# Kernel tuning notes

Hardware: AMD Instinct MI355X
Metric: run time of the kernel (lower is better)

Reference implementation:

```python
import jax, jax.numpy as jnp
import numpy as np

N_HEAD = 16
N_EMBD = 1024
SEQ = 2048
BATCH = 4


def setup_inputs() -> dict:
    key = jax.random.key(0)
    ks = jax.random.split(key, 5)
    s_in = 1.0 / np.sqrt(N_EMBD)
    return {
        "x": jax.random.normal(ks[0], (BATCH, SEQ, N_EMBD), dtype=jnp.float32),
        "W_attn": jax.random.normal(ks[1], (N_EMBD, 3 * N_EMBD), dtype=jnp.float32) * s_in,
        "b_attn": jax.random.normal(ks[2], (3 * N_EMBD,), dtype=jnp.float32) * 0.01,
        "W_proj": jax.random.normal(ks[3], (N_EMBD, N_EMBD), dtype=jnp.float32) * s_in,
        "b_proj": jax.random.normal(ks[4], (N_EMBD,), dtype=jnp.float32) * 0.01,
    }


def reference(x, W_attn, b_attn, W_proj, b_proj):
    B, T, C = x.shape
    H = N_HEAD
    D = C // H  # head dim
    qkv = x @ W_attn + b_attn                      # [B,T,3C]
    q, k, v = jnp.split(qkv, 3, axis=-1)
    # [B,T,C] -> [B,H,T,D]
    q = q.reshape(B, T, H, D).transpose(0, 2, 1, 3)
    k = k.reshape(B, T, H, D).transpose(0, 2, 1, 3)
    v = v.reshape(B, T, H, D).transpose(0, 2, 1, 3)
    scale = 1.0 / np.sqrt(D).astype(np.float32)
    att = jnp.einsum('bhqd,bhkd->bhqk', q, k) * scale   # [B,H,T,T]
    causal = jnp.tril(jnp.ones((T, T), dtype=bool))
    att = jnp.where(causal, att, jnp.finfo(att.dtype).min)
    att = jax.nn.softmax(att, axis=-1)
    y = jnp.einsum('bhqk,bhkd->bhqd', att, v)            # [B,H,T,D]
    y = y.transpose(0, 2, 1, 3).reshape(B, T, C)
    return y @ W_proj + b_proj
```

## Files before the change

kernel.cpp:

```cpp
#include <hip/hip_runtime.h>
#include <stdint.h>

typedef __attribute__((ext_vector_type(8))) short short8;
typedef __attribute__((ext_vector_type(4))) short short4v;
typedef __attribute__((ext_vector_type(4))) float f32x4;
typedef __attribute__((ext_vector_type(2))) unsigned int uint2v;

#define B_ 4
#define T_ 2048
#define C_ 1024
#define H_ 16
#define D_ 64
#define C3_ 3072

#define AS1 __attribute__((address_space(1)))
#define AS3 __attribute__((address_space(3)))

#define QK_SCALE 0.18033688f

__device__ __forceinline__ unsigned short f2bf(float f) {
    union { float f; uint32_t u; } v; v.f = f;
    uint32_t r = v.u + 0x7FFFu + ((v.u >> 16) & 1u);
    return (unsigned short)(r >> 16);
}

__device__ __forceinline__ uint32_t pk_bf16(float lo, float hi) {
    uint32_t r;
    asm("v_cvt_pk_bf16_f32 %0, %1, %2" : "=v"(r) : "v"(lo), "v"(hi));
    return r;
}

__global__ void k_cvt_bf16(const float* __restrict__ in, unsigned short* __restrict__ out, int n4) {
    int i = blockIdx.x * blockDim.x + threadIdx.x;
    if (i >= n4) return;
    float4 v = ((const float4*)in)[i];
    unsigned short o0 = f2bf(v.x), o1 = f2bf(v.y), o2 = f2bf(v.z), o3 = f2bf(v.w);
    unsigned long long packed = (unsigned long long)o0 | ((unsigned long long)o1 << 16)
        | ((unsigned long long)o2 << 32) | ((unsigned long long)o3 << 48);
    *(unsigned long long*)(out + (size_t)i * 4) = packed;
}

__global__ void k_wtrans(const float* __restrict__ W, unsigned short* __restrict__ WT, int K, int N) {
    __shared__ float t[32][33];
    int n0 = blockIdx.x * 32, k0 = blockIdx.y * 32;
    int tx = threadIdx.x, ty = threadIdx.y;
#pragma unroll
    for (int i = 0; i < 4; ++i)
        t[ty + i * 8][tx] = W[(size_t)(k0 + ty + i * 8) * N + n0 + tx];
    __syncthreads();
#pragma unroll
    for (int i = 0; i < 4; ++i)
        WT[(size_t)(n0 + ty + i * 8) * K + k0 + tx] = f2bf(t[tx][ty + i * 8]);
}

__global__ void k_prep_vt(const unsigned short* __restrict__ qkv, unsigned short* __restrict__ vt) {
    int bh = blockIdx.y; int b = bh >> 4, h = bh & 15;
    int t0 = blockIdx.x * 64;
    __shared__ unsigned short tile[64][72];
    int tid = threadIdx.x;
    int r = tid >> 3;
    int c = (tid & 7) * 8;
#pragma unroll
    for (int rr = 0; rr < 64; rr += 32) {
        const unsigned short* src = qkv + (size_t)(b * T_ + t0 + r + rr) * C3_ + 2 * C_ + h * D_ + c;
        short8 v = *(const short8*)src;
#pragma unroll
        for (int j = 0; j < 8; ++j) tile[r + rr][c + j] = (unsigned short)v[j];
    }
    __syncthreads();
#pragma unroll
    for (int rr = 0; rr < 64; rr += 32) {
        int d = r + rr;
        short8 sv;
#pragma unroll
        for (int j = 0; j < 8; ++j) sv[j] = (short)tile[c + j][d];
        *(short8*)(vt + (size_t)bh * D_ * T_ + (size_t)d * T_ + t0 + c) = sv;
    }
}

template<bool OUT_BF16>
__global__ __launch_bounds__(512) void k_gemm_bt(const unsigned short* __restrict__ A,
                                                 const unsigned short* __restrict__ BT,
                                                 const float* __restrict__ bias,
                                                 unsigned short* __restrict__ outb,
                                                 float* __restrict__ outf,
                                                 int M, int N, int K) {
    __shared__ __align__(16) char arena[147456];
    int tid = threadIdx.x;
    int w = tid >> 6, lane = tid & 63;
    int wrow = w >> 1, wcol = w & 1;
    int m0 = blockIdx.y * 256, n0 = blockIdx.x * 128;
    int lr = lane & 15, lg = lane >> 4;

    f32x4 acc[4][4] = {};

    int gr = tid >> 3;
    int scb = ((tid & 7) << 4) ^ (((tid >> 3) & 7) << 4);
    const char* sA[4];
    const char* sB[2];
#pragma unroll
    for (int r = 0; r < 4; ++r)
        sA[r] = (const char*)A + (size_t)(m0 + gr + r * 64) * K * 2 + scb;
#pragma unroll
    for (int r = 0; r < 2; ++r)
        sB[r] = (const char*)BT + (size_t)(n0 + gr + r * 64) * K * 2 + scb;

    int inner = (lg * 16) ^ ((lr & 7) << 4);
    int aoff = wrow * 8192 + lr * 128 + inner;
    int boff = 32768 + wcol * 8192 + lr * 128 + inner;

#define GSTAGE(OFS)                                                                                 \
    {                                                                                               \
        _Pragma("unroll")                                                                           \
        for (int r = 0; r < 4; ++r) {                                                               \
            __builtin_amdgcn_global_load_lds((const AS1 void*)sA[r],                                \
                (AS3 void*)(arena + (OFS) + tid * 16 + r * 8192), 16, 0, 0);                        \
            sA[r] += 128;                                                                           \
        }                                                                                           \
        _Pragma("unroll")                                                                           \
        for (int r = 0; r < 2; ++r) {                                                               \
            __builtin_amdgcn_global_load_lds((const AS1 void*)sB[r],                                \
                (AS3 void*)(arena + (OFS) + 32768 + tid * 16 + r * 8192), 16, 0, 0);                \
            sB[r] += 128;                                                                           \
        }                                                                                           \
    }

#define GCOMPUTE(OFS)                                                                               \
    {                                                                                               \
        short8 af[4][2], bf[4][2];                                                                  \
        _Pragma("unroll")                                                                           \
        for (int i = 0; i < 4; ++i) {                                                               \
            int addrA = (OFS) + aoff + i * 2048;                                                    \
            af[i][0] = *(const short8*)(arena + addrA);                                             \
            af[i][1] = *(const short8*)(arena + (addrA ^ 64));                                      \
        }                                                                                           \
        _Pragma("unroll")                                                                           \
        for (int j = 0; j < 4; ++j) {                                                               \
            int addrB = (OFS) + boff + j * 2048;                                                    \
            bf[j][0] = *(const short8*)(arena + addrB);                                             \
            bf[j][1] = *(const short8*)(arena + (addrB ^ 64));                                      \
        }                                                                                           \
        __builtin_amdgcn_s_setprio(1);                                                              \
        _Pragma("unroll")                                                                           \
        for (int i = 0; i < 4; ++i)                                                                 \
            _Pragma("unroll")                                                                       \
            for (int j = 0; j < 4; ++j) {                                                           \
                acc[i][j] = __builtin_amdgcn_mfma_f32_16x16x32_bf16(af[i][0], bf[j][0], acc[i][j], 0, 0, 0); \
                acc[i][j] = __builtin_amdgcn_mfma_f32_16x16x32_bf16(af[i][1], bf[j][1], acc[i][j], 0, 0, 0); \
            }                                                                                       \
        __builtin_amdgcn_s_setprio(0);                                                              \
    }

    int NT = K >> 6;
    int ofs0 = 0, ofs1 = 49152, ofs2 = 98304;

    GSTAGE(ofs0);
    GSTAGE(ofs1);
    asm volatile("s_waitcnt vmcnt(6)" ::: "memory");
    __builtin_amdgcn_s_barrier();
    __builtin_amdgcn_sched_barrier(0);

    for (int t = 0; t < NT; ++t) {
        bool pf = (t + 2 < NT);
        if (pf) GSTAGE(ofs2);
        GCOMPUTE(ofs0);
        if (pf) { asm volatile("s_waitcnt vmcnt(6)" ::: "memory"); }
        else    { asm volatile("s_waitcnt vmcnt(0)" ::: "memory"); }
        __builtin_amdgcn_s_barrier();
        __builtin_amdgcn_sched_barrier(0);
        int tmp = ofs0; ofs0 = ofs1; ofs1 = ofs2; ofs2 = tmp;
    }
#undef GSTAGE
#undef GCOMPUTE

#pragma unroll
    for (int i = 0; i < 4; ++i) {
        int row = m0 + wrow * 64 + i * 16 + lg * 4;
#pragma unroll
        for (int j = 0; j < 4; ++j) {
            int col = n0 + wcol * 64 + j * 16 + lr;
            float bv = bias[col];
#pragma unroll
            for (int r = 0; r < 4; ++r) {
                float v = acc[i][j][r] + bv;
                if (OUT_BF16) {
                    if (col < C_) v *= QK_SCALE;
                    outb[(size_t)(row + r) * N + col] = f2bf(v);
                } else {
                    outf[(size_t)(row + r) * N + col] = v;
                }
            }
        }
    }
}

__global__ __launch_bounds__(256, 4) void k_attn(const unsigned short* __restrict__ qkv,
                                                 const unsigned short* __restrict__ vt,
                                                 unsigned short* __restrict__ y) {
    __shared__ __align__(16) char arena[40960];
    int tid = threadIdx.x;
    int w = tid >> 6, lane = tid & 63;
    int lr = lane & 15, lg = lane >> 4;

    int bid = blockIdx.x;
    int bid2 = (bid & 7) * 128 + (bid >> 3);
    int bh = bid2 >> 4, pair = bid2 & 15;
    int b = bh >> 4, h = bh & 15;

    const unsigned short* kbase = qkv + (size_t)(b * T_) * C3_ + C_ + h * D_;
    const unsigned short* vtb = vt + (size_t)bh * D_ * T_;

    int sw_ = (lr & 7) << 4;
    int RB0 = lr * 128 + ((lg * 16) ^ sw_);
    int RB1 = RB0 ^ 64;
    int jl = (lr >> 1) & 3;
    int pbase = 32768 + w * 2048 + lr * 128
              + ((((lg >> 1) ^ (lr & 1)) << 4) | (((lg & 1) ^ (lr >> 3)) << 3));
    int pwa[4];
#pragma unroll
    for (int j = 0; j < 4; ++j) pwa[j] = pbase + ((j ^ jl) << 5);
    int prd0 = 32768 + w * 2048 + lr * 128 + ((lg ^ (lr & 7)) << 4);
    int prd1 = prd0 ^ 64;
    int hs = lr & 8;
    int prA0a = prd0 + hs,       prA0b = prd0 + (8 ^ hs);
    int prA1a = prd1 + hs,       prA1b = prd1 + (8 ^ hs);

    int row0 = tid >> 3, row1 = 32 + (tid >> 3);
    int scol0 = ((tid & 7) << 4) ^ ((row0 & 7) << 4);
    int scol1 = ((tid & 7) << 4) ^ ((row1 & 7) << 4);

    const char *sK0, *sK1, *sV0, *sV1;

#define ASTAGE(LDSOFF)                                                                                  \
    {                                                                                                   \
        __builtin_amdgcn_global_load_lds((const AS1 void*)sK0, (AS3 void*)(arena + (LDSOFF) + w * 1024), 16, 0, 0);          \
        __builtin_amdgcn_global_load_lds((const AS1 void*)sK1, (AS3 void*)(arena + (LDSOFF) + 4096 + w * 1024), 16, 0, 0);   \
        __builtin_amdgcn_global_load_lds((const AS1 void*)sV0, (AS3 void*)(arena + 16384 + (LDSOFF) + w * 1024), 16, 0, 0);  \
        __builtin_amdgcn_global_load_lds((const AS1 void*)sV1, (AS3 void*)(arena + 16384 + (LDSOFF) + 4096 + w * 1024), 16, 0, 0); \
        sK0 += 64 * C3_ * 2; sK1 += 64 * C3_ * 2; sV0 += 128; sV1 += 128;                               \
    }

#define ACOMPUTE(LDSOFF, KT)                                                                            \
    {                                                                                                   \
        f32x4 s[4];                                                                                     \
        __builtin_amdgcn_s_setprio(1);                                                                  \
        _Pragma("unroll")                                                                               \
        for (int j = 0; j < 4; ++j) {                                                                   \
            short8 kf0 = *(const short8*)(arena + RB0 + (LDSOFF) + j * 2048);                           \
            short8 kf1 = *(const short8*)(arena + RB1 + (LDSOFF) + j * 2048);                           \
            f32x4 z = {};                                                                               \
            z = __builtin_amdgcn_mfma_f32_16x16x32_bf16(kf0, qf0, z, 0, 0, 0);                          \
            s[j] = __builtin_amdgcn_mfma_f32_16x16x32_bf16(kf1, qf1, z, 0, 0, 0);                       \
        }                                                                                               \
        __builtin_amdgcn_s_setprio(0);                                                                  \
        if ((KT) == ntiles - 1) {                                                                       \
            int kb = (KT) * 64 + lg * 4 - qv;                                                           \
            _Pragma("unroll")                                                                           \
            for (int j = 0; j < 4; ++j)                                                                 \
                _Pragma("unroll")                                                                       \
                for (int r = 0; r < 4; ++r)                                                             \
                    if (kb + j * 16 + r > 0) s[j][r] = -INFINITY;                                       \
        }                                                                                               \
        _Pragma("unroll")                                                                               \
        for (int j = 0; j < 4; ++j)                                                                     \
            _Pragma("unroll")                                                                           \
            for (int r = 0; r < 4; ++r) {                                                               \
                float pv = __builtin_amdgcn_exp2f(s[j][r]);                                             \
                s[j][r] = pv;                                                                           \
                ls += pv;                                                                               \
            }                                                                                           \
        _Pragma("unroll")                                                                               \
        for (int j = 0; j < 4; ++j) {                                                                   \
            uint2v W;                                                                                   \
            W[0] = pk_bf16(s[j][0], s[j][1]);                                                           \
            W[1] = pk_bf16(s[j][2], s[j][3]);                                                           \
            *(uint2v*)(arena + pwa[j]) = W;                                                             \
        }                                                                                               \
        short4v l0 = *(const short4v*)(arena + prA0a);                                                  \
        short4v h0 = *(const short4v*)(arena + prA0b);                                                  \
        short4v l1 = *(const short4v*)(arena + prA1a);                                                  \
        short4v h1 = *(const short4v*)(arena + prA1b);                                                  \
        short8 pa0 = __builtin_shufflevector(l0, h0, 0, 1, 2, 3, 4, 5, 6, 7);                           \
        short8 pa1 = __builtin_shufflevector(l1, h1, 0, 1, 2, 3, 4, 5, 6, 7);                           \
        __builtin_amdgcn_s_setprio(1);                                                                  \
        _Pragma("unroll")                                                                               \
        for (int dt = 0; dt < 4; ++dt) {                                                                \
            short8 vf0 = *(const short8*)(arena + RB0 + 16384 + (LDSOFF) + dt * 2048);                  \
            short8 vf1 = *(const short8*)(arena + RB1 + 16384 + (LDSOFF) + dt * 2048);                  \
            o[dt] = __builtin_amdgcn_mfma_f32_16x16x32_bf16(pa0, vf0, o[dt], 0, 0, 0);                  \
            o[dt] = __builtin_amdgcn_mfma_f32_16x16x32_bf16(pa1, vf1, o[dt], 0, 0, 0);                  \
        }                                                                                               \
        __builtin_amdgcn_s_setprio(0);                                                                  \
    }

#pragma unroll 1
    for (int half = 0; half < 2; ++half) {
        int qt = half ? (31 - pair) : pair;
        int q0 = qt * 64;
        int ntiles = qt + 1;

        const unsigned short* qrow = qkv + (size_t)(b * T_ + q0 + w * 16 + lr) * C3_ + h * D_;
        short8 qf0 = *(const short8*)(qrow + lg * 8);
        short8 qf1 = *(const short8*)(qrow + 32 + lg * 8);

        f32x4 o[4] = {};
        float ls = 0.f;
        int qv = q0 + w * 16 + lr;

        sK0 = (const char*)(kbase + (size_t)row0 * C3_) + scol0;
        sK1 = (const char*)(kbase + (size_t)row1 * C3_) + scol1;
        sV0 = (const char*)(vtb + (size_t)row0 * T_) + scol0;
        sV1 = (const char*)(vtb + (size_t)row1 * T_) + scol1;

        ASTAGE(0);
        asm volatile("s_waitcnt vmcnt(0)" ::: "memory");
        __syncthreads();

#pragma unroll 1
        for (int kt = 0; kt < ntiles; kt += 2) {
            if (kt + 1 < ntiles) ASTAGE(8192);
            ACOMPUTE(0, kt);
            asm volatile("s_waitcnt vmcnt(0)" ::: "memory");
            __syncthreads();
            if (kt + 1 < ntiles) {
                if (kt + 2 < ntiles) ASTAGE(0);
                ACOMPUTE(8192, kt + 1);
                asm volatile("s_waitcnt vmcnt(0)" ::: "memory");
                __syncthreads();
            }
        }

        ls += __shfl_xor(ls, 16);
        ls += __shfl_xor(ls, 32);
#pragma unroll
        for (int r = 0; r < 4; ++r) {
            float lst = __shfl(ls, lg * 4 + r, 64);
            float inv = 1.0f / lst;
            int q = q0 + w * 16 + lg * 4 + r;
            unsigned short* yrow = y + (size_t)(b * T_ + q) * C_ + h * D_;
#pragma unroll
            for (int dt = 0; dt < 4; ++dt)
                yrow[dt * 16 + lr] = f2bf(o[dt][r] * inv);
        }
    }
#undef ASTAGE
#undef ACOMPUTE
}

extern "C" void kernel_launch(void* const* d_in, const int* in_sizes, int n_in,
                              void* d_out, int out_size, void* d_ws, size_t ws_size,
                              hipStream_t stream) {
    const float* x  = (const float*)d_in[0];
    const float* Wa = (const float*)d_in[1];
    const float* ba = (const float*)d_in[2];
    const float* Wp = (const float*)d_in[3];
    const float* bp = (const float*)d_in[4];
    float* out = (float*)d_out;

    char* ws = (char*)d_ws;
    unsigned short* xb  = (unsigned short*)(ws);
    unsigned short* wat = (unsigned short*)(ws + 16777216);
    unsigned short* wpt = (unsigned short*)(ws + 23068672);
    unsigned short* qkv = (unsigned short*)(ws + 25165824);
    unsigned short* vt  = (unsigned short*)(ws + 75497472);
    unsigned short* y   = xb;

    k_cvt_bf16<<<8192, 256, 0, stream>>>(x, xb, (B_ * T_ * C_) / 4);
    k_wtrans<<<dim3(C3_ / 32, C_ / 32), dim3(32, 8), 0, stream>>>(Wa, wat, C_, C3_);
    k_wtrans<<<dim3(C_ / 32, C_ / 32), dim3(32, 8), 0, stream>>>(Wp, wpt, C_, C_);
    k_gemm_bt<true><<<dim3(C3_ / 128, (B_ * T_) / 256), 512, 0, stream>>>(
        xb, wat, ba, qkv, nullptr, B_ * T_, C3_, C_);
    k_prep_vt<<<dim3(T_ / 64, B_ * H_), 256, 0, stream>>>(qkv, vt);
    k_attn<<<1024, 256, 0, stream>>>(qkv, vt, y);
    k_gemm_bt<false><<<dim3(C_ / 128, (B_ * T_) / 256), 512, 0, stream>>>(
        y, wpt, bp, nullptr, out, B_ * T_, C_, C_);
}
```

Baseline: 168.0 us.

## Restructure GEMM to 4 waves with BK=32 tiles for two blocks per CU

The projection GEMM kernel now runs 256 threads (4 waves) instead of 8, with each wave computing a 128x64 output sub-tile (8x4 MFMA accumulators). The K-step drops from 64 to 32, which halves the triple-buffered LDS arena to 72KB so two blocks can be resident per CU. The LDS swizzle and staging addresses are adjusted to match the narrower rows. The aim is better latency hiding through two co-resident blocks. In exchange it doubles the number of K iterations and barriers and raises accumulator register pressure per thread.

```diff
diff --git a/kernel.cpp b/kernel.cpp
--- a/kernel.cpp
+++ b/kernel.cpp
@@ -79,80 +79,72 @@
 }
 
 template<bool OUT_BF16>
-__global__ __launch_bounds__(512) void k_gemm_bt(const unsigned short* __restrict__ A,
-                                                 const unsigned short* __restrict__ BT,
-                                                 const float* __restrict__ bias,
-                                                 unsigned short* __restrict__ outb,
-                                                 float* __restrict__ outf,
-                                                 int M, int N, int K) {
-    __shared__ __align__(16) char arena[147456];
+__global__ __launch_bounds__(256, 2) void k_gemm_bt(const unsigned short* __restrict__ A,
+                                                    const unsigned short* __restrict__ BT,
+                                                    const float* __restrict__ bias,
+                                                    unsigned short* __restrict__ outb,
+                                                    float* __restrict__ outf,
+                                                    int M, int N, int K) {
+    __shared__ __align__(16) char arena[73728];
     int tid = threadIdx.x;
     int w = tid >> 6, lane = tid & 63;
     int wrow = w >> 1, wcol = w & 1;
     int m0 = blockIdx.y * 256, n0 = blockIdx.x * 128;
     int lr = lane & 15, lg = lane >> 4;
 
-    f32x4 acc[4][4] = {};
-
-    int gr = tid >> 3;
-    int scb = ((tid & 7) << 4) ^ (((tid >> 3) & 7) << 4);
+    f32x4 acc[8][4] = {};
+
+    int grow = tid >> 2;
+    int scb = ((tid & 3) << 4) ^ (((tid >> 2) & 3) << 4);
     const char* sA[4];
     const char* sB[2];
 #pragma unroll
-    for (int r = 0; r < 4; ++r)
-        sA[r] = (const char*)A + (size_t)(m0 + gr + r * 64) * K * 2 + scb;
-#pragma unroll
-    for (int r = 0; r < 2; ++r)
-        sB[r] = (const char*)BT + (size_t)(n0 + gr + r * 64) * K * 2 + scb;
-
-    int inner = (lg * 16) ^ ((lr & 7) << 4);
-    int aoff = wrow * 8192 + lr * 128 + inner;
-    int boff = 32768 + wcol * 8192 + lr * 128 + inner;
+    for (int rr = 0; rr < 4; ++rr)
+        sA[rr] = (const char*)A + (size_t)(m0 + grow + rr * 64) * K * 2 + scb;
+#pragma unroll
+    for (int rr = 0; rr < 2; ++rr)
+        sB[rr] = (const char*)BT + (size_t)(n0 + grow + rr * 64) * K * 2 + scb;
+
+    int inner = (lg * 16) ^ ((lr & 3) << 4);
+    int aoff = wrow * 8192 + lr * 64 + inner;
+    int boff = 16384 + wcol * 4096 + lr * 64 + inner;
 
 #define GSTAGE(OFS)                                                                                 \
     {                                                                                               \
         _Pragma("unroll")                                                                           \
-        for (int r = 0; r < 4; ++r) {                                                               \
-            __builtin_amdgcn_global_load_lds((const AS1 void*)sA[r],                                \
-                (AS3 void*)(arena + (OFS) + tid * 16 + r * 8192), 16, 0, 0);                        \
-            sA[r] += 128;                                                                           \
+        for (int rr = 0; rr < 4; ++rr) {                                                            \
+            __builtin_amdgcn_global_load_lds((const AS1 void*)sA[rr],                               \
+                (AS3 void*)(arena + (OFS) + tid * 16 + rr * 4096), 16, 0, 0);                       \
+            sA[rr] += 64;                                                                           \
         }                                                                                           \
         _Pragma("unroll")                                                                           \
-        for (int r = 0; r < 2; ++r) {                                                               \
-            __builtin_amdgcn_global_load_lds((const AS1 void*)sB[r],                                \
-                (AS3 void*)(arena + (OFS) + 32768 + tid * 16 + r * 8192), 16, 0, 0);                \
-            sB[r] += 128;                                                                           \
+        for (int rr = 0; rr < 2; ++rr) {                                                            \
+            __builtin_amdgcn_global_load_lds((const AS1 void*)sB[rr],                               \
+                (AS3 void*)(arena + (OFS) + 16384 + tid * 16 + rr * 4096), 16, 0, 0);               \
+            sB[rr] += 64;                                                                           \
         }                                                                                           \
     }
 
 #define GCOMPUTE(OFS)                                                                               \
     {                                                                                               \
-        short8 af[4][2], bf[4][2];                                                                  \
-        _Pragma("unroll")                                                                           \
-        for (int i = 0; i < 4; ++i) {                                                               \
-            int addrA = (OFS) + aoff + i * 2048;                                                    \
-            af[i][0] = *(const short8*)(arena + addrA);                                             \
-            af[i][1] = *(const short8*)(arena + (addrA ^ 64));                                      \
-        }                                                                                           \
-        _Pragma("unroll")                                                                           \
-        for (int j = 0; j < 4; ++j) {                                                               \
-            int addrB = (OFS) + boff + j * 2048;                                                    \
-            bf[j][0] = *(const short8*)(arena + addrB);                                             \
-            bf[j][1] = *(const short8*)(arena + (addrB ^ 64));                                      \
-        }                                                                                           \
+        short8 af[8], bf[4];                                                                        \
+        _Pragma("unroll")                                                                           \
+        for (int i = 0; i < 8; ++i)                                                                 \
+            af[i] = *(const short8*)(arena + (OFS) + aoff + i * 1024);                              \
+        _Pragma("unroll")                                                                           \
+        for (int j = 0; j < 4; ++j)                                                                 \
+            bf[j] = *(const short8*)(arena + (OFS) + boff + j * 1024);                              \
         __builtin_amdgcn_s_setprio(1);                                                              \
         _Pragma("unroll")                                                                           \
-        for (int i = 0; i < 4; ++i)                                                                 \
+        for (int i = 0; i < 8; ++i)                                                                 \
             _Pragma("unroll")                                                                       \
-            for (int j = 0; j < 4; ++j) {                                                           \
-                acc[i][j] = __builtin_amdgcn_mfma_f32_16x16x32_bf16(af[i][0], bf[j][0], acc[i][j], 0, 0, 0); \
-                acc[i][j] = __builtin_amdgcn_mfma_f32_16x16x32_bf16(af[i][1], bf[j][1], acc[i][j], 0, 0, 0); \
-            }                                                                                       \
+            for (int j = 0; j < 4; ++j)                                                             \
+                acc[i][j] = __builtin_amdgcn_mfma_f32_16x16x32_bf16(af[i], bf[j], acc[i][j], 0, 0, 0); \
         __builtin_amdgcn_s_setprio(0);                                                              \
     }
 
-    int NT = K >> 6;
-    int ofs0 = 0, ofs1 = 49152, ofs2 = 98304;
+    int NT = K >> 5;
+    int ofs0 = 0, ofs1 = 24576, ofs2 = 49152;
 
     GSTAGE(ofs0);
     GSTAGE(ofs1);
@@ -174,8 +166,8 @@
 #undef GCOMPUTE
 
 #pragma unroll
-    for (int i = 0; i < 4; ++i) {
-        int row = m0 + wrow * 64 + i * 16 + lg * 4;
+    for (int i = 0; i < 8; ++i) {
+        int row = m0 + wrow * 128 + i * 16 + lg * 4;
 #pragma unroll
         for (int j = 0; j < 4; ++j) {
             int col = n0 + wcol * 64 + j * 16 + lr;
@@ -368,10 +360,10 @@
     k_cvt_bf16<<<8192, 256, 0, stream>>>(x, xb, (B_ * T_ * C_) / 4);
     k_wtrans<<<dim3(C3_ / 32, C_ / 32), dim3(32, 8), 0, stream>>>(Wa, wat, C_, C3_);
     k_wtrans<<<dim3(C_ / 32, C_ / 32), dim3(32, 8), 0, stream>>>(Wp, wpt, C_, C_);
-    k_gemm_bt<true><<<dim3(C3_ / 128, (B_ * T_) / 256), 512, 0, stream>>>(
+    k_gemm_bt<true><<<dim3(C3_ / 128, (B_ * T_) / 256), 256, 0, stream>>>(
         xb, wat, ba, qkv, nullptr, B_ * T_, C3_, C_);
     k_prep_vt<<<dim3(T_ / 64, B_ * H_), 256, 0, stream>>>(qkv, vt);
     k_attn<<<1024, 256, 0, stream>>>(qkv, vt, y);
-    k_gemm_bt<false><<<dim3(C_ / 128, (B_ * T_) / 256), 512, 0, stream>>>(
+    k_gemm_bt<false><<<dim3(C_ / 128, (B_ * T_) / 256), 256, 0, stream>>>(
         y, wpt, bp, nullptr, out, B_ * T_, C_, C_);
 }
```

New measurement: 166.0 us. Within noise of the previous version (-1.2%).

## Interleave GEMM loads and MFMAs in phased pipeline with block swizzle

Applied to the files above, without the earlier changes.

Restructures the GEMM main loop into four phases that each issue part of the next stage's global-to-LDS loads, then a few LDS fragment reads, then eight MFMAs, with workgroup barriers between phases. This replaces the load-everything-then-compute pattern and is meant to overlap memory traffic with matrix math. It also remaps block indices in an 8-way interleaved order to improve L2 locality, and sets launch_bounds min-blocks to 2. The extra barriers add sync overhead. The min-blocks hint may be unattainable given the 144KB LDS arena per block.

```diff
diff --git a/kernel.cpp b/kernel.cpp
--- a/kernel.cpp
+++ b/kernel.cpp
@@ -79,17 +79,24 @@
 }
 
 template<bool OUT_BF16>
-__global__ __launch_bounds__(512) void k_gemm_bt(const unsigned short* __restrict__ A,
-                                                 const unsigned short* __restrict__ BT,
-                                                 const float* __restrict__ bias,
-                                                 unsigned short* __restrict__ outb,
-                                                 float* __restrict__ outf,
-                                                 int M, int N, int K) {
+__global__ __launch_bounds__(512, 2) void k_gemm_bt(const unsigned short* __restrict__ A,
+                                                    const unsigned short* __restrict__ BT,
+                                                    const float* __restrict__ bias,
+                                                    unsigned short* __restrict__ outb,
+                                                    float* __restrict__ outf,
+                                                    int M, int N, int K) {
     __shared__ __align__(16) char arena[147456];
     int tid = threadIdx.x;
     int w = tid >> 6, lane = tid & 63;
     int wrow = w >> 1, wcol = w & 1;
-    int m0 = blockIdx.y * 256, n0 = blockIdx.x * 128;
+
+    int lin = blockIdx.y * gridDim.x + blockIdx.x;
+    int nwg8 = (gridDim.x * gridDim.y) >> 3;
+    int newlin = (lin & 7) * nwg8 + (lin >> 3);
+    int bx = newlin % gridDim.x;
+    int by = newlin / gridDim.x;
+    int m0 = by * 256, n0 = bx * 128;
+
     int lr = lane & 15, lg = lane >> 4;
 
     f32x4 acc[4][4] = {};
@@ -99,79 +106,91 @@
     const char* sA[4];
     const char* sB[2];
 #pragma unroll
-    for (int r = 0; r < 4; ++r)
-        sA[r] = (const char*)A + (size_t)(m0 + gr + r * 64) * K * 2 + scb;
-#pragma unroll
-    for (int r = 0; r < 2; ++r)
-        sB[r] = (const char*)BT + (size_t)(n0 + gr + r * 64) * K * 2 + scb;
+    for (int rr = 0; rr < 4; ++rr)
+        sA[rr] = (const char*)A + (size_t)(m0 + gr + rr * 64) * K * 2 + scb;
+#pragma unroll
+    for (int rr = 0; rr < 2; ++rr)
+        sB[rr] = (const char*)BT + (size_t)(n0 + gr + rr * 64) * K * 2 + scb;
 
     int inner = (lg * 16) ^ ((lr & 7) << 4);
     int aoff = wrow * 8192 + lr * 128 + inner;
     int boff = 32768 + wcol * 8192 + lr * 128 + inner;
 
-#define GSTAGE(OFS)                                                                                 \
+#define GLA(OFS, R) { __builtin_amdgcn_global_load_lds((const AS1 void*)sA[R],                      \
+                        (AS3 void*)(arena + (OFS) + tid * 16 + (R) * 8192), 16, 0, 0);              \
+                      sA[R] += 128; }
+#define GLB(OFS, R) { __builtin_amdgcn_global_load_lds((const AS1 void*)sB[R],                      \
+                        (AS3 void*)(arena + (OFS) + 32768 + tid * 16 + (R) * 8192), 16, 0, 0);      \
+                      sB[R] += 128; }
+#define LDA(OFS, I, KH) (*(const short8*)(arena + (((OFS) + aoff + (I) * 2048) ^ ((KH) * 64))))
+#define LDB(OFS, J, KH) (*(const short8*)(arena + (((OFS) + boff + (J) * 2048) ^ ((KH) * 64))))
+#define MFMA8(I0, I1, RA0, RA1)                                                                     \
     {                                                                                               \
-        _Pragma("unroll")                                                                           \
-        for (int r = 0; r < 4; ++r) {                                                               \
-            __builtin_amdgcn_global_load_lds((const AS1 void*)sA[r],                                \
-                (AS3 void*)(arena + (OFS) + tid * 16 + r * 8192), 16, 0, 0);                        \
-            sA[r] += 128;                                                                           \
-        }                                                                                           \
-        _Pragma("unroll")                                                                           \
-        for (int r = 0; r < 2; ++r) {                                                               \
-            __builtin_amdgcn_global_load_lds((const AS1 void*)sB[r],                                \
-                (AS3 void*)(arena + (OFS) + 32768 + tid * 16 + r * 8192), 16, 0, 0);                \
-            sB[r] += 128;                                                                           \
-        }                                                                                           \
-    }
-
-#define GCOMPUTE(OFS)                                                                               \
-    {                                                                                               \
-        short8 af[4][2], bf[4][2];                                                                  \
-        _Pragma("unroll")                                                                           \
-        for (int i = 0; i < 4; ++i) {                                                               \
-            int addrA = (OFS) + aoff + i * 2048;                                                    \
-            af[i][0] = *(const short8*)(arena + addrA);                                             \
-            af[i][1] = *(const short8*)(arena + (addrA ^ 64));                                      \
-        }                                                                                           \
-        _Pragma("unroll")                                                                           \
-        for (int j = 0; j < 4; ++j) {                                                               \
-            int addrB = (OFS) + boff + j * 2048;                                                    \
-            bf[j][0] = *(const short8*)(arena + addrB);                                             \
-            bf[j][1] = *(const short8*)(arena + (addrB ^ 64));                                      \
-        }                                                                                           \
         __builtin_amdgcn_s_setprio(1);                                                              \
-        _Pragma("unroll")                                                                           \
-        for (int i = 0; i < 4; ++i)                                                                 \
-            _Pragma("unroll")                                                                       \
-            for (int j = 0; j < 4; ++j) {                                                           \
-                acc[i][j] = __builtin_amdgcn_mfma_f32_16x16x32_bf16(af[i][0], bf[j][0], acc[i][j], 0, 0, 0); \
-                acc[i][j] = __builtin_amdgcn_mfma_f32_16x16x32_bf16(af[i][1], bf[j][1], acc[i][j], 0, 0, 0); \
-            }                                                                                       \
+        acc[I0][0] = __builtin_amdgcn_mfma_f32_16x16x32_bf16(RA0, rb0, acc[I0][0], 0, 0, 0);        \
+        acc[I0][1] = __builtin_amdgcn_mfma_f32_16x16x32_bf16(RA0, rb1, acc[I0][1], 0, 0, 0);        \
+        acc[I0][2] = __builtin_amdgcn_mfma_f32_16x16x32_bf16(RA0, rb2, acc[I0][2], 0, 0, 0);        \
+        acc[I0][3] = __builtin_amdgcn_mfma_f32_16x16x32_bf16(RA0, rb3, acc[I0][3], 0, 0, 0);        \
+        acc[I1][0] = __builtin_amdgcn_mfma_f32_16x16x32_bf16(RA1, rb0, acc[I1][0], 0, 0, 0);        \
+        acc[I1][1] = __builtin_amdgcn_mfma_f32_16x16x32_bf16(RA1, rb1, acc[I1][1], 0, 0, 0);        \
+        acc[I1][2] = __builtin_amdgcn_mfma_f32_16x16x32_bf16(RA1, rb2, acc[I1][2], 0, 0, 0);        \
+        acc[I1][3] = __builtin_amdgcn_mfma_f32_16x16x32_bf16(RA1, rb3, acc[I1][3], 0, 0, 0);        \
         __builtin_amdgcn_s_setprio(0);                                                              \
     }
 
     int NT = K >> 6;
     int ofs0 = 0, ofs1 = 49152, ofs2 = 98304;
 
-    GSTAGE(ofs0);
-    GSTAGE(ofs1);
+    GLA(ofs0, 0) GLA(ofs0, 1) GLA(ofs0, 2) GLA(ofs0, 3) GLB(ofs0, 0) GLB(ofs0, 1)
+    GLA(ofs1, 0) GLA(ofs1, 1) GLA(ofs1, 2) GLA(ofs1, 3) GLB(ofs1, 0) GLB(ofs1, 1)
     asm volatile("s_waitcnt vmcnt(6)" ::: "memory");
     __builtin_amdgcn_s_barrier();
-    __builtin_amdgcn_sched_barrier(0);
 
     for (int t = 0; t < NT; ++t) {
         bool pf = (t + 2 < NT);
-        if (pf) GSTAGE(ofs2);
-        GCOMPUTE(ofs0);
-        if (pf) { asm volatile("s_waitcnt vmcnt(6)" ::: "memory"); }
-        else    { asm volatile("s_waitcnt vmcnt(0)" ::: "memory"); }
-        __builtin_amdgcn_s_barrier();
-        __builtin_amdgcn_sched_barrier(0);
+        short8 rb0, rb1, rb2, rb3;
+        if (pf) { GLA(ofs2, 0) GLA(ofs2, 1) }
+        {
+            short8 ra0 = LDA(ofs0, 0, 0), ra1 = LDA(ofs0, 1, 0);
+            rb0 = LDB(ofs0, 0, 0); rb1 = LDB(ofs0, 1, 0); rb2 = LDB(ofs0, 2, 0); rb3 = LDB(ofs0, 3, 0);
+            __builtin_amdgcn_s_barrier();
+            asm volatile("s_waitcnt lgkmcnt(0)" ::: "memory");
+            MFMA8(0, 1, ra0, ra1)
+            __builtin_amdgcn_s_barrier();
+        }
+        if (pf) { GLA(ofs2, 2) GLA(ofs2, 3) }
+        {
+            short8 ra0 = LDA(ofs0, 2, 0), ra1 = LDA(ofs0, 3, 0);
+            __builtin_amdgcn_s_barrier();
+            asm volatile("s_waitcnt lgkmcnt(0)" ::: "memory");
+            MFMA8(2, 3, ra0, ra1)
+            __builtin_amdgcn_s_barrier();
+        }
+        if (pf) { GLB(ofs2, 0) GLB(ofs2, 1) }
+        {
+            short8 ra0 = LDA(ofs0, 0, 1), ra1 = LDA(ofs0, 1, 1);
+            rb0 = LDB(ofs0, 0, 1); rb1 = LDB(ofs0, 1, 1); rb2 = LDB(ofs0, 2, 1); rb3 = LDB(ofs0, 3, 1);
+            __builtin_amdgcn_s_barrier();
+            asm volatile("s_waitcnt lgkmcnt(0)" ::: "memory");
+            MFMA8(0, 1, ra0, ra1)
+            __builtin_amdgcn_s_barrier();
+        }
+        {
+            short8 ra0 = LDA(ofs0, 2, 1), ra1 = LDA(ofs0, 3, 1);
+            if (pf) { asm volatile("s_waitcnt vmcnt(6)" ::: "memory"); }
+            else    { asm volatile("s_waitcnt vmcnt(0)" ::: "memory"); }
+            __builtin_amdgcn_s_barrier();
+            asm volatile("s_waitcnt lgkmcnt(0)" ::: "memory");
+            MFMA8(2, 3, ra0, ra1)
+            __builtin_amdgcn_s_barrier();
+        }
         int tmp = ofs0; ofs0 = ofs1; ofs1 = ofs2; ofs2 = tmp;
     }
-#undef GSTAGE
-#undef GCOMPUTE
+#undef GLA
+#undef GLB
+#undef LDA
+#undef LDB
+#undef MFMA8
 
 #pragma unroll
     for (int i = 0; i < 4; ++i) {
```

New measurement: 170.1 us. Within noise of the previous version (+1.2%).
